# Kernel tuning notes

Measured on AMD Instinct MI355X. Metric: run time of the kernel, lower is better.

The kernel has to match this reference:

```python
import jax, jax.numpy as jnp
from jax import lax
import numpy as np

B, T, D, H, O = 256, 512, 512, 1024, 512

def setup_inputs() -> dict:
    key = jax.random.key(0)
    k1, k2, k3, k4 = jax.random.split(key, 4)
    return {
        "x": jax.random.normal(k1, (B, T, D), dtype=jnp.float32),
        "h0": jnp.zeros((B, H), dtype=jnp.float32),
        "w_xh": jax.random.normal(k2, (D, H), dtype=jnp.float32) * 0.05,
        "w_hh": jax.random.normal(k3, (H, H), dtype=jnp.float32) * 0.05,
        "w_hy": jax.random.normal(k4, (H, O), dtype=jnp.float32) * 0.05,
    }

def reference(x, h0, w_xh, w_hh, w_hy):
    # x: [B, T, D] -> scan over time. Each step matches MyRNNCell.call:
    #   h' = tanh(x_t @ W_xh + h @ W_hh);  y_t = h' @ W_hy
    xT = jnp.swapaxes(x, 0, 1)  # [T, B, D]
    def step(h, xt):
        h_next = jnp.tanh(xt @ w_xh + h @ w_hh)  # [B, H]
        return h_next, h_next @ w_hy             # output [B, O]
    h_final, outs = lax.scan(step, h0, xT)
    return jnp.swapaxes(outs, 0, 1), h_final  # [B, T, O], [B, H]
```

## Files before the change

### kernel.cpp

```cpp
#include <hip/hip_runtime.h>
#include <hip/hip_bf16.h>

#define BB 256
#define TT 512
#define DD 512
#define HH 1024
#define OO 512

typedef unsigned short u16;
typedef unsigned int u32;
typedef unsigned long long u64;
typedef __attribute__((ext_vector_type(8))) short frag8;
typedef __attribute__((ext_vector_type(4))) float floatx4;

#define MFMA16 __builtin_amdgcn_mfma_f32_16x16x32_bf16
#define AL(p) __hip_atomic_load((p), __ATOMIC_RELAXED, __HIP_MEMORY_SCOPE_AGENT)
#define AS(p, v) __hip_atomic_store((p), (v), __ATOMIC_RELAXED, __HIP_MEMORY_SCOPE_AGENT)

__device__ __forceinline__ u16 f2b(float f) {
  union { float f; u32 u; } v; v.f = f;
  u32 r = v.u + 0x7fffu + ((v.u >> 16) & 1u);
  return (u16)(r >> 16);
}
__device__ __forceinline__ float b2f(u16 b) {
  union { u32 u; float f; } v; v.u = ((u32)b) << 16; return v.f;
}
__device__ __forceinline__ float fast_tanh(float x) {
  float e = __expf(2.0f * x);
  return 1.0f - 2.0f / (e + 1.0f);
}
__device__ __forceinline__ frag8 mkfrag(u64 lo, u64 hi) {
  union { u64 d[2]; frag8 f; } u; u.d[0] = lo; u.d[1] = hi; return u.f;
}
__device__ __forceinline__ u32 cvtpk(float lo, float hi) {
  u32 r;
  asm("v_cvt_pk_bf16_f32 %0, %1, %2" : "=v"(r) : "v"(lo), "v"(hi));
  return r;
}
__device__ __forceinline__ frag8 cvt8(float4 a, float4 b) {
  union { u32 w[4]; frag8 f; } u;
  u.w[0] = cvtpk(a.x, a.y); u.w[1] = cvtpk(a.z, a.w);
  u.w[2] = cvtpk(b.x, b.y); u.w[3] = cvtpk(b.z, b.w);
  return u.f;
}

__global__ void k_transpose(const float* __restrict__ src, u16* __restrict__ dst,
                            int K, int N) {
  int idx = blockIdx.x * 256 + threadIdx.x;
  if (idx >= K * N) return;
  int k = idx / N, n = idx - k * N;
  dst[(u64)n * K + k] = f2b(src[idx]);
}

__global__ void k_init_s0(const float* __restrict__ h0, u16* __restrict__ S) {
  int idx = blockIdx.x * 256 + threadIdx.x;
  if (idx < BB * HH) S[idx] = f2b(h0[idx]);
}

__global__ void k_final_h(const u16* __restrict__ Sl, float* __restrict__ out) {
  int idx = blockIdx.x * 256 + threadIdx.x;
  if (idx < BB * HH) out[idx] = b2f(Sl[idx]);
}

__global__ void k_fill_sent(uint4* __restrict__ p) {
  u64 i = (u64)blockIdx.x * 256 + threadIdx.x;
  p[i] = make_uint4(0xFFFFFFFFu, 0xFFFFFFFFu, 0xFFFFFFFFu, 0xFFFFFFFFu);
}

__global__ __launch_bounds__(256) void k_scan(const u16* __restrict__ Whh_t,
                                              const u16* __restrict__ Wxh_t,
                                              const float* __restrict__ X,
                                              u16* __restrict__ S) {
  extern __shared__ __align__(16) u16 smem[];
  u16* Ws = smem;
  u16* Wxs = smem + 32 * 1032;
  float* Red = (float*)(smem + 32 * 1032 + 32 * 520);

  const int tid = threadIdx.x;
  const int mb = blockIdx.x;
  const int nb = blockIdx.y;
  const int m0 = mb * 32, n0 = nb * 32;
  const int lane = tid & 63, wv = tid >> 6;
  const int fr = lane & 15, q = lane >> 4;
  const int kbase = wv * 256;
  const int xkbase = wv * 128;
  const int er = tid >> 4;
  const int ec = (tid & 15) * 2;

  {
    const u16* Wb = Whh_t + (u64)n0 * HH;
#pragma unroll
    for (int it = 0; it < 16; ++it) {
      int linear = (it * 256 + tid) * 8;
      int r = linear >> 10, c = linear & 1023;
      *(uint4*)&Ws[r * 1032 + c] = *(const uint4*)(Wb + (u64)r * HH + c);
    }
  }
  {
    const u16* Wb = Wxh_t + (u64)n0 * DD;
#pragma unroll
    for (int it = 0; it < 8; ++it) {
      int linear = (it * 256 + tid) * 8;
      int r = linear >> 9, c = linear & 511;
      *(uint4*)&Wxs[r * 520 + c] = *(const uint4*)(Wb + (u64)r * DD + c);
    }
  }
  __syncthreads();

  for (int t = 0; t < TT; ++t) {
    const float* xr0 = X + ((u64)(m0 + fr) * TT + t) * DD + xkbase;
    const float* xr1 = X + ((u64)(m0 + 16 + fr) * TT + t) * DD + xkbase;
    float4 xv[16];
#pragma unroll
    for (int xkt = 0; xkt < 4; ++xkt) {
      xv[xkt * 4 + 0] = *(const float4*)(xr0 + xkt * 32 + q * 8);
      xv[xkt * 4 + 1] = *(const float4*)(xr0 + xkt * 32 + q * 8 + 4);
      xv[xkt * 4 + 2] = *(const float4*)(xr1 + xkt * 32 + q * 8);
      xv[xkt * 4 + 3] = *(const float4*)(xr1 + xkt * 32 + q * 8 + 4);
    }

    floatx4 acc[2][2];
#pragma unroll
    for (int i = 0; i < 2; ++i)
#pragma unroll
      for (int j = 0; j < 2; ++j) acc[i][j] = (floatx4){0.f, 0.f, 0.f, 0.f};

#pragma unroll
    for (int xkt = 0; xkt < 4; ++xkt) {
      const int k = xkbase + xkt * 32 + q * 8;
      frag8 ax0 = cvt8(xv[xkt * 4 + 0], xv[xkt * 4 + 1]);
      frag8 ax1 = cvt8(xv[xkt * 4 + 2], xv[xkt * 4 + 3]);
      frag8 b0 = *(const frag8*)&Wxs[fr * 520 + k];
      frag8 b1 = *(const frag8*)&Wxs[(16 + fr) * 520 + k];
      acc[0][0] = MFMA16(ax0, b0, acc[0][0], 0, 0, 0);
      acc[0][1] = MFMA16(ax0, b1, acc[0][1], 0, 0, 0);
      acc[1][0] = MFMA16(ax1, b0, acc[1][0], 0, 0, 0);
      acc[1][1] = MFMA16(ax1, b1, acc[1][1], 0, 0, 0);
    }

    const u16* St = S + (u64)t * BB * HH;
    const u64* A0p = (const u64*)(St + (u64)(m0 + fr) * HH + kbase + q * 8);
    const u64* A1p = (const u64*)(St + (u64)(m0 + 16 + fr) * HH + kbase + q * 8);
#pragma unroll
    for (int kt = 0; kt < 8; ++kt) {
      u64 c0, c1, c2, c3;
      for (;;) {
        c0 = AL(A0p + kt * 8);     c1 = AL(A0p + kt * 8 + 1);
        c2 = AL(A1p + kt * 8);     c3 = AL(A1p + kt * 8 + 1);
        u32 bad = ((u32)c0 == 0xFFFFFFFFu) | ((u32)(c0 >> 32) == 0xFFFFFFFFu) |
                  ((u32)c1 == 0xFFFFFFFFu) | ((u32)(c1 >> 32) == 0xFFFFFFFFu) |
                  ((u32)c2 == 0xFFFFFFFFu) | ((u32)(c2 >> 32) == 0xFFFFFFFFu) |
                  ((u32)c3 == 0xFFFFFFFFu) | ((u32)(c3 >> 32) == 0xFFFFFFFFu);
        if (!bad) break;
      }
      const int k = kbase + kt * 32 + q * 8;
      frag8 b0 = *(const frag8*)&Ws[fr * 1032 + k];
      frag8 b1 = *(const frag8*)&Ws[(16 + fr) * 1032 + k];
      frag8 af0 = mkfrag(c0, c1);
      frag8 af1 = mkfrag(c2, c3);
      acc[0][0] = MFMA16(af0, b0, acc[0][0], 0, 0, 0);
      acc[0][1] = MFMA16(af0, b1, acc[0][1], 0, 0, 0);
      acc[1][0] = MFMA16(af1, b0, acc[1][0], 0, 0, 0);
      acc[1][1] = MFMA16(af1, b1, acc[1][1], 0, 0, 0);
    }

    float* R = Red + (t & 1) * (4 * 32 * 33);
#pragma unroll
    for (int im = 0; im < 2; ++im)
#pragma unroll
      for (int in = 0; in < 2; ++in)
#pragma unroll
        for (int r = 0; r < 4; ++r) {
          int row = im * 16 + q * 4 + r;
          int col = in * 16 + fr;
          R[(wv * 32 + row) * 33 + col] = acc[im][in][r];
        }
    __syncthreads();

    u16* Sout = S + (u64)(t + 1) * BB * HH + (u64)m0 * HH + n0;
    float s00 = R[(0 * 32 + er) * 33 + ec]     + R[(1 * 32 + er) * 33 + ec] +
                R[(2 * 32 + er) * 33 + ec]     + R[(3 * 32 + er) * 33 + ec];
    float s01 = R[(0 * 32 + er) * 33 + ec + 1] + R[(1 * 32 + er) * 33 + ec + 1] +
                R[(2 * 32 + er) * 33 + ec + 1] + R[(3 * 32 + er) * 33 + ec + 1];
    float s10 = R[(0 * 32 + er + 16) * 33 + ec]     + R[(1 * 32 + er + 16) * 33 + ec] +
                R[(2 * 32 + er + 16) * 33 + ec]     + R[(3 * 32 + er + 16) * 33 + ec];
    float s11 = R[(0 * 32 + er + 16) * 33 + ec + 1] + R[(1 * 32 + er + 16) * 33 + ec + 1] +
                R[(2 * 32 + er + 16) * 33 + ec + 1] + R[(3 * 32 + er + 16) * 33 + ec + 1];
    u32 p0 = cvtpk(fast_tanh(s00), fast_tanh(s01));
    u32 p1 = cvtpk(fast_tanh(s10), fast_tanh(s11));
    AS((u32*)(Sout + (u64)er * HH + ec), p0);
    AS((u32*)(Sout + (u64)(er + 16) * HH + ec), p1);
  }
}

__global__ __launch_bounds__(256) void k_gemm_hy(const u16* __restrict__ Hs,
                                                 const u16* __restrict__ Wt,
                                                 float* __restrict__ out) {
  __shared__ __align__(16) u16 As[64 * 72];
  __shared__ __align__(16) u16 Bs[64 * 72];
  const int tid = threadIdx.x;
  const int m0 = blockIdx.x * 64, n0 = blockIdx.y * 64;
  const int lane = tid & 63, wv = tid >> 6;
  const int fr = lane & 15, quad = lane >> 4;

  floatx4 acc[4];
#pragma unroll
  for (int i = 0; i < 4; ++i) acc[i] = (floatx4){0.f, 0.f, 0.f, 0.f};

  for (int kc = 0; kc < HH; kc += 64) {
    const u16* Ab = Hs + (u64)m0 * HH + kc;
#pragma unroll
    for (int it = 0; it < 2; ++it) {
      int linear = (it * 256 + tid) * 8;
      int r = linear >> 6, c = linear & 63;
      *(uint4*)&As[r * 72 + c] = *(const uint4*)(Ab + (u64)r * HH + c);
    }
    const u16* Bb = Wt + (u64)n0 * HH + kc;
#pragma unroll
    for (int it = 0; it < 2; ++it) {
      int linear = (it * 256 + tid) * 8;
      int n = linear >> 6, c = linear & 63;
      *(uint4*)&Bs[n * 72 + c] = *(const uint4*)(Bb + (u64)n * HH + c);
    }
    __syncthreads();
#pragma unroll
    for (int kk = 0; kk < 64; kk += 32) {
      frag8 bf = *(const frag8*)&Bs[(wv * 16 + fr) * 72 + kk + quad * 8];
#pragma unroll
      for (int i = 0; i < 4; ++i) {
        frag8 af = *(const frag8*)&As[(i * 16 + fr) * 72 + kk + quad * 8];
        acc[i] = MFMA16(af, bf, acc[i], 0, 0, 0);
      }
    }
    __syncthreads();
  }
  const int col = n0 + wv * 16 + fr;
#pragma unroll
  for (int i = 0; i < 4; ++i) {
#pragma unroll
    for (int r = 0; r < 4; ++r) {
      int m = m0 + i * 16 + quad * 4 + r;
      int t = m >> 8;
      int b = m & (BB - 1);
      out[(u64)b * (TT * OO) + (u64)t * OO + col] = acc[i][r];
    }
  }
}

extern "C" void kernel_launch(void* const* d_in, const int* in_sizes, int n_in,
                              void* d_out, int out_size, void* d_ws, size_t ws_size,
                              hipStream_t stream) {
  (void)in_sizes; (void)n_in; (void)out_size; (void)ws_size;
  const float* x    = (const float*)d_in[0];
  const float* h0   = (const float*)d_in[1];
  const float* w_xh = (const float*)d_in[2];
  const float* w_hh = (const float*)d_in[3];
  const float* w_hy = (const float*)d_in[4];
  float* out = (float*)d_out;

  u16* S = (u16*)d_ws;
  u64 s_elems = (u64)(TT + 1) * BB * HH;
  u16* Wxh_t = S + s_elems;
  u16* Whh_t = Wxh_t + (u64)HH * DD;
  u16* Why_t = Whh_t + (u64)HH * HH;

  k_transpose<<<dim3((DD * HH + 255) / 256), dim3(256), 0, stream>>>(w_xh, Wxh_t, DD, HH);
  k_transpose<<<dim3((HH * HH + 255) / 256), dim3(256), 0, stream>>>(w_hh, Whh_t, HH, HH);
  k_transpose<<<dim3((HH * OO + 255) / 256), dim3(256), 0, stream>>>(w_hy, Why_t, HH, OO);
  k_init_s0<<<dim3(BB * HH / 256), dim3(256), 0, stream>>>(h0, S);

  k_fill_sent<<<dim3(65536), dim3(256), 0, stream>>>(
      (uint4*)(S + (u64)BB * HH));

  const int scan_lds = 32 * 1032 * 2 + 32 * 520 * 2 + 2 * 4 * 32 * 33 * 4;
  hipFuncSetAttribute((const void*)k_scan,
                      hipFuncAttributeMaxDynamicSharedMemorySize, scan_lds);
  k_scan<<<dim3(8, 32), dim3(256), scan_lds, stream>>>(Whh_t, Wxh_t, x, S);

  k_gemm_hy<<<dim3((TT * BB) / 64, OO / 64), dim3(256), 0, stream>>>(
      S + (u64)BB * HH, Why_t, out);
  k_final_h<<<dim3(BB * HH / 256), dim3(256), 0, stream>>>(
      S + (u64)TT * BB * HH, out + (u64)BB * TT * OO);
}
```

Baseline: 4.060 ms.

## Prefetch next-step x and issue all hidden-state loads before spin-check in RNN loop

The recurrent kernel now issues all 16 atomic loads of the previous hidden-state slice at once, then checks readiness and re-polls only if any sentinel is still present, instead of spinning per k-tile. It also prefetches the x rows for step t+1 into a second register buffer while computing step t, unrolling the time loop by two with ping-pong buffers. This is meant to hide global load latency on the serial per-step critical path. The extra register buffers raise register pressure, which could spill or reduce occupancy.

```diff
diff --git a/kernel.cpp b/kernel.cpp
--- a/kernel.cpp
+++ b/kernel.cpp
@@ -107,90 +107,120 @@
   }
   __syncthreads();
 
-  for (int t = 0; t < TT; ++t) {
-    const float* xr0 = X + ((u64)(m0 + fr) * TT + t) * DD + xkbase;
-    const float* xr1 = X + ((u64)(m0 + 16 + fr) * TT + t) * DD + xkbase;
-    float4 xv[16];
-#pragma unroll
-    for (int xkt = 0; xkt < 4; ++xkt) {
-      xv[xkt * 4 + 0] = *(const float4*)(xr0 + xkt * 32 + q * 8);
-      xv[xkt * 4 + 1] = *(const float4*)(xr0 + xkt * 32 + q * 8 + 4);
-      xv[xkt * 4 + 2] = *(const float4*)(xr1 + xkt * 32 + q * 8);
-      xv[xkt * 4 + 3] = *(const float4*)(xr1 + xkt * 32 + q * 8 + 4);
-    }
-
-    floatx4 acc[2][2];
-#pragma unroll
-    for (int i = 0; i < 2; ++i)
-#pragma unroll
-      for (int j = 0; j < 2; ++j) acc[i][j] = (floatx4){0.f, 0.f, 0.f, 0.f};
-
-#pragma unroll
-    for (int xkt = 0; xkt < 4; ++xkt) {
-      const int k = xkbase + xkt * 32 + q * 8;
-      frag8 ax0 = cvt8(xv[xkt * 4 + 0], xv[xkt * 4 + 1]);
-      frag8 ax1 = cvt8(xv[xkt * 4 + 2], xv[xkt * 4 + 3]);
-      frag8 b0 = *(const frag8*)&Wxs[fr * 520 + k];
-      frag8 b1 = *(const frag8*)&Wxs[(16 + fr) * 520 + k];
-      acc[0][0] = MFMA16(ax0, b0, acc[0][0], 0, 0, 0);
-      acc[0][1] = MFMA16(ax0, b1, acc[0][1], 0, 0, 0);
-      acc[1][0] = MFMA16(ax1, b0, acc[1][0], 0, 0, 0);
-      acc[1][1] = MFMA16(ax1, b1, acc[1][1], 0, 0, 0);
-    }
-
-    const u16* St = S + (u64)t * BB * HH;
-    const u64* A0p = (const u64*)(St + (u64)(m0 + fr) * HH + kbase + q * 8);
-    const u64* A1p = (const u64*)(St + (u64)(m0 + 16 + fr) * HH + kbase + q * 8);
-#pragma unroll
-    for (int kt = 0; kt < 8; ++kt) {
-      u64 c0, c1, c2, c3;
-      for (;;) {
-        c0 = AL(A0p + kt * 8);     c1 = AL(A0p + kt * 8 + 1);
-        c2 = AL(A1p + kt * 8);     c3 = AL(A1p + kt * 8 + 1);
-        u32 bad = ((u32)c0 == 0xFFFFFFFFu) | ((u32)(c0 >> 32) == 0xFFFFFFFFu) |
-                  ((u32)c1 == 0xFFFFFFFFu) | ((u32)(c1 >> 32) == 0xFFFFFFFFu) |
-                  ((u32)c2 == 0xFFFFFFFFu) | ((u32)(c2 >> 32) == 0xFFFFFFFFu) |
-                  ((u32)c3 == 0xFFFFFFFFu) | ((u32)(c3 >> 32) == 0xFFFFFFFFu);
-        if (!bad) break;
-      }
-      const int k = kbase + kt * 32 + q * 8;
-      frag8 b0 = *(const frag8*)&Ws[fr * 1032 + k];
-      frag8 b1 = *(const frag8*)&Ws[(16 + fr) * 1032 + k];
-      frag8 af0 = mkfrag(c0, c1);
-      frag8 af1 = mkfrag(c2, c3);
-      acc[0][0] = MFMA16(af0, b0, acc[0][0], 0, 0, 0);
-      acc[0][1] = MFMA16(af0, b1, acc[0][1], 0, 0, 0);
-      acc[1][0] = MFMA16(af1, b0, acc[1][0], 0, 0, 0);
-      acc[1][1] = MFMA16(af1, b1, acc[1][1], 0, 0, 0);
-    }
-
-    float* R = Red + (t & 1) * (4 * 32 * 33);
-#pragma unroll
-    for (int im = 0; im < 2; ++im)
-#pragma unroll
-      for (int in = 0; in < 2; ++in)
-#pragma unroll
-        for (int r = 0; r < 4; ++r) {
-          int row = im * 16 + q * 4 + r;
-          int col = in * 16 + fr;
-          R[(wv * 32 + row) * 33 + col] = acc[im][in][r];
-        }
-    __syncthreads();
-
-    u16* Sout = S + (u64)(t + 1) * BB * HH + (u64)m0 * HH + n0;
-    float s00 = R[(0 * 32 + er) * 33 + ec]     + R[(1 * 32 + er) * 33 + ec] +
-                R[(2 * 32 + er) * 33 + ec]     + R[(3 * 32 + er) * 33 + ec];
-    float s01 = R[(0 * 32 + er) * 33 + ec + 1] + R[(1 * 32 + er) * 33 + ec + 1] +
-                R[(2 * 32 + er) * 33 + ec + 1] + R[(3 * 32 + er) * 33 + ec + 1];
-    float s10 = R[(0 * 32 + er + 16) * 33 + ec]     + R[(1 * 32 + er + 16) * 33 + ec] +
-                R[(2 * 32 + er + 16) * 33 + ec]     + R[(3 * 32 + er + 16) * 33 + ec];
-    float s11 = R[(0 * 32 + er + 16) * 33 + ec + 1] + R[(1 * 32 + er + 16) * 33 + ec + 1] +
-                R[(2 * 32 + er + 16) * 33 + ec + 1] + R[(3 * 32 + er + 16) * 33 + ec + 1];
-    u32 p0 = cvtpk(fast_tanh(s00), fast_tanh(s01));
-    u32 p1 = cvtpk(fast_tanh(s10), fast_tanh(s11));
-    AS((u32*)(Sout + (u64)er * HH + ec), p0);
-    AS((u32*)(Sout + (u64)(er + 16) * HH + ec), p1);
-  }
+#define XLOAD(t_, xv_)                                                        \
+  do {                                                                        \
+    int tc_ = (t_) < TT ? (t_) : TT - 1;                                      \
+    const float* xr0_ = X + ((u64)(m0 + fr) * TT + tc_) * DD + xkbase;        \
+    const float* xr1_ = X + ((u64)(m0 + 16 + fr) * TT + tc_) * DD + xkbase;   \
+    _Pragma("unroll") for (int xkt = 0; xkt < 4; ++xkt) {                     \
+      xv_[xkt * 4 + 0] = *(const float4*)(xr0_ + xkt * 32 + q * 8);           \
+      xv_[xkt * 4 + 1] = *(const float4*)(xr0_ + xkt * 32 + q * 8 + 4);       \
+      xv_[xkt * 4 + 2] = *(const float4*)(xr1_ + xkt * 32 + q * 8);           \
+      xv_[xkt * 4 + 3] = *(const float4*)(xr1_ + xkt * 32 + q * 8 + 4);       \
+    }                                                                         \
+  } while (0)
+
+#define STEP(t_, P_, XC_, XN_)                                                \
+  do {                                                                        \
+                               \
+    const u16* St_ = S + (u64)(t_) * BB * HH;                                 \
+    const u64* A0p_ = (const u64*)(St_ + (u64)(m0 + fr) * HH + kbase + q * 8);\
+    const u64* A1p_ =                                                         \
+        (const u64*)(St_ + (u64)(m0 + 16 + fr) * HH + kbase + q * 8);         \
+    u64 ha_[16], hb_[16];                                                     \
+    _Pragma("unroll") for (int kt = 0; kt < 8; ++kt) {                        \
+      ha_[2 * kt] = AL(A0p_ + kt * 8);                                        \
+      ha_[2 * kt + 1] = AL(A0p_ + kt * 8 + 1);                                \
+      hb_[2 * kt] = AL(A1p_ + kt * 8);                                        \
+      hb_[2 * kt + 1] = AL(A1p_ + kt * 8 + 1);                                \
+    }                                                                         \
+                  \
+    XLOAD((t_) + 1, XN_);                                                     \
+    floatx4 acc_[2][2];                                                       \
+    _Pragma("unroll") for (int i = 0; i < 2; ++i)                             \
+        _Pragma("unroll") for (int j = 0; j < 2; ++j)                         \
+            acc_[i][j] = (floatx4){0.f, 0.f, 0.f, 0.f};                       \
+                    \
+    _Pragma("unroll") for (int xkt = 0; xkt < 4; ++xkt) {                     \
+      const int k_ = xkbase + xkt * 32 + q * 8;                               \
+      frag8 ax0_ = cvt8(XC_[xkt * 4 + 0], XC_[xkt * 4 + 1]);                  \
+      frag8 ax1_ = cvt8(XC_[xkt * 4 + 2], XC_[xkt * 4 + 3]);                  \
+      frag8 b0_ = *(const frag8*)&Wxs[fr * 520 + k_];                         \
+      frag8 b1_ = *(const frag8*)&Wxs[(16 + fr) * 520 + k_];                  \
+      acc_[0][0] = MFMA16(ax0_, b0_, acc_[0][0], 0, 0, 0);                    \
+      acc_[0][1] = MFMA16(ax0_, b1_, acc_[0][1], 0, 0, 0);                    \
+      acc_[1][0] = MFMA16(ax1_, b0_, acc_[1][0], 0, 0, 0);                    \
+      acc_[1][1] = MFMA16(ax1_, b1_, acc_[1][1], 0, 0, 0);                    \
+    }                                                                         \
+         \
+    for (;;) {                                                                \
+      u32 bad_ = 0;                                                           \
+      _Pragma("unroll") for (int i = 0; i < 16; ++i) {                        \
+        bad_ |= ((u32)ha_[i] == 0xFFFFFFFFu) |                                \
+                ((u32)(ha_[i] >> 32) == 0xFFFFFFFFu) |                        \
+                ((u32)hb_[i] == 0xFFFFFFFFu) |                                \
+                ((u32)(hb_[i] >> 32) == 0xFFFFFFFFu);                         \
+      }                                                                       \
+      if (!bad_) break;                                                       \
+      _Pragma("unroll") for (int kt = 0; kt < 8; ++kt) {                      \
+        ha_[2 * kt] = AL(A0p_ + kt * 8);                                      \
+        ha_[2 * kt + 1] = AL(A0p_ + kt * 8 + 1);                              \
+        hb_[2 * kt] = AL(A1p_ + kt * 8);                                      \
+        hb_[2 * kt + 1] = AL(A1p_ + kt * 8 + 1);                              \
+      }                                                                       \
+    }                                                                         \
+                                                              \
+    _Pragma("unroll") for (int kt = 0; kt < 8; ++kt) {                        \
+      const int k_ = kbase + kt * 32 + q * 8;                                 \
+      frag8 b0_ = *(const frag8*)&Ws[fr * 1032 + k_];                         \
+      frag8 b1_ = *(const frag8*)&Ws[(16 + fr) * 1032 + k_];                  \
+      frag8 af0_ = mkfrag(ha_[2 * kt], ha_[2 * kt + 1]);                      \
+      frag8 af1_ = mkfrag(hb_[2 * kt], hb_[2 * kt + 1]);                      \
+      acc_[0][0] = MFMA16(af0_, b0_, acc_[0][0], 0, 0, 0);                    \
+      acc_[0][1] = MFMA16(af0_, b1_, acc_[0][1], 0, 0, 0);                    \
+      acc_[1][0] = MFMA16(af1_, b0_, acc_[1][0], 0, 0, 0);                    \
+      acc_[1][1] = MFMA16(af1_, b1_, acc_[1][1], 0, 0, 0);                    \
+    }                                                                         \
+        \
+    float* R_ = Red + (P_) * (4 * 32 * 33);                                   \
+    _Pragma("unroll") for (int im = 0; im < 2; ++im)                          \
+        _Pragma("unroll") for (int in = 0; in < 2; ++in)                      \
+            _Pragma("unroll") for (int r = 0; r < 4; ++r) {                   \
+      int row_ = im * 16 + q * 4 + r;                                         \
+      int col_ = in * 16 + fr;                                                \
+      R_[(wv * 32 + row_) * 33 + col_] = acc_[im][in][r];                     \
+    }                                                                         \
+    __syncthreads();                                                          \
+                       \
+    u16* Sout_ = S + (u64)((t_) + 1) * BB * HH + (u64)m0 * HH + n0;           \
+    float s00_ = R_[(0 * 32 + er) * 33 + ec] + R_[(1 * 32 + er) * 33 + ec] +  \
+                 R_[(2 * 32 + er) * 33 + ec] + R_[(3 * 32 + er) * 33 + ec];   \
+    float s01_ =                                                              \
+        R_[(0 * 32 + er) * 33 + ec + 1] + R_[(1 * 32 + er) * 33 + ec + 1] +   \
+        R_[(2 * 32 + er) * 33 + ec + 1] + R_[(3 * 32 + er) * 33 + ec + 1];    \
+    float s10_ = R_[(0 * 32 + er + 16) * 33 + ec] +                           \
+                 R_[(1 * 32 + er + 16) * 33 + ec] +                           \
+                 R_[(2 * 32 + er + 16) * 33 + ec] +                           \
+                 R_[(3 * 32 + er + 16) * 33 + ec];                            \
+    float s11_ = R_[(0 * 32 + er + 16) * 33 + ec + 1] +                       \
+                 R_[(1 * 32 + er + 16) * 33 + ec + 1] +                       \
+                 R_[(2 * 32 + er + 16) * 33 + ec + 1] +                       \
+                 R_[(3 * 32 + er + 16) * 33 + ec + 1];                        \
+    u32 p0_ = cvtpk(fast_tanh(s00_), fast_tanh(s01_));                        \
+    u32 p1_ = cvtpk(fast_tanh(s10_), fast_tanh(s11_));                        \
+    AS((u32*)(Sout_ + (u64)er * HH + ec), p0_);                               \
+    AS((u32*)(Sout_ + (u64)(er + 16) * HH + ec), p1_);                        \
+  } while (0)
+
+  float4 xvA[16], xvB[16];
+  XLOAD(0, xvA);
+
+  for (int tb = 0; tb < TT; tb += 2) {
+    STEP(tb, 0, xvA, xvB);
+    STEP(tb + 1, 1, xvB, xvA);
+  }
+#undef STEP
+#undef XLOAD
 }
 
 __global__ __launch_bounds__(256) void k_gemm_hy(const u16* __restrict__ Hs,
```

Result: slower. 5.685 ms (+40.0%).
